# Kernel optimization log

Measured on AMD Instinct MI355X. Metric: run time of the kernel, lower is better.

## Reference

```python
import jax, jax.numpy as jnp
import numpy as np


def setup_inputs() -> dict:
    key = jax.random.key(0)
    k1, k2, k3, k4 = jax.random.split(key, 4)
    T, H, I, E, K = 4096, 1024, 1024, 8, 2
    hidden_states = jax.random.normal(k1, (T, H), dtype=jnp.float32)
    router_logits = jax.random.normal(k2, (T, E), dtype=jnp.float32)
    # fused gate+up projection: [E, H, 2*I]; down projection: [E, I, H]
    up_weight = jax.random.normal(k3, (E, H, 2 * I), dtype=jnp.float32) * 0.02
    down_weight = jax.random.normal(k4, (E, I, H), dtype=jnp.float32) * 0.02
    return {"hidden_states": hidden_states, "router_logits": router_logits,
            "up_weight": up_weight, "down_weight": down_weight, "topk": K}


def reference(hidden_states, router_logits, up_weight, down_weight, topk):
    T, H = hidden_states.shape
    E = up_weight.shape[0]
    I = down_weight.shape[1]
    K = topk
    # select_experts: softmax over all experts, top-k, renormalize weights
    probs = jax.nn.softmax(router_logits, axis=-1)
    topk_w, topk_ids = jax.lax.top_k(probs, K)               # [T, K]
    topk_w = topk_w / jnp.sum(topk_w, axis=-1, keepdims=True)
    # expand tokens: each token is dispatched K times (grouped-GEMM operand)
    xk = jnp.repeat(hidden_states, K, axis=0)                # [T*K, H]
    flat_ids = topk_ids.reshape(-1)                          # [T*K]
    acc = jnp.zeros((T * K, H), dtype=hidden_states.dtype)
    for e in range(E):  # fixed small expert loop (grouped GEMM semantics)
        mask = (flat_ids == e).astype(hidden_states.dtype)[:, None]
        xe = xk * mask                                       # zero out non-e tokens
        gu = xe @ up_weight[e]                               # [T*K, 2I]
        h = jax.nn.silu(gu[:, :I]) * gu[:, I:]               # gated SiLU
        acc = acc + h @ down_weight[e]                       # [T*K, H]
    # combine: weighted sum over the K expert slots (reduce step)
    out = jnp.einsum('tk,tkh->th', topk_w, acc.reshape(T, K, H))
    return out
```

## Files before the change

### kernel.cpp

```cpp
#include <hip/hip_runtime.h>
#include <hip/hip_bf16.h>


#define T_TOK 4096
#define HDIM  1024
#define NEXP  8
#define RROWS (T_TOK * 2)
#define MAXPE T_TOK

typedef unsigned short u16;
typedef short v8s __attribute__((ext_vector_type(8)));
typedef float v4f __attribute__((ext_vector_type(4)));
typedef __attribute__((address_space(3))) unsigned int as3_u32;
typedef const __attribute__((address_space(1))) unsigned int as1_u32c;

__device__ __forceinline__ float b2f(u16 u) {
    union { unsigned int i; float f; } v; v.i = ((unsigned int)u) << 16; return v.f;
}
__device__ __forceinline__ u16 f2b(float f) {
    union { float f; unsigned int i; } v; v.f = f;
    unsigned int x = v.i;
    return (u16)((x + 0x7FFFu + ((x >> 16) & 1u)) >> 16);
}
__device__ __forceinline__ unsigned int pack2(float a, float b) {
    return (unsigned int)f2b(a) | ((unsigned int)f2b(b) << 16);
}
__device__ __forceinline__ void stage16(const u16* g, u16* l) {
    __builtin_amdgcn_global_load_lds((as1_u32c*)g, (as3_u32*)l, 16, 0, 0);
}

__device__ __forceinline__ void cvt_tile(const float* __restrict__ Wb,
                                         u16* __restrict__ Wtb,
                                         int N, int n0b, int k0b, u16* sm) {
    const int tid = threadIdx.x;
    const int m = tid & 15, rr = tid >> 4;
    float4 f[16];
#pragma unroll
    for (int s = 0; s < 4; s++)
#pragma unroll
        for (int j = 0; j < 4; j++)
            f[s * 4 + j] = *(const float4*)(Wb + (size_t)(k0b + s * 64 + rr * 4 + j) * N
                                               + n0b + m * 4);
#pragma unroll
    for (int s = 0; s < 4; s++) {
        const int kc = s * 16 + rr;
        const float* fp = (const float*)&f[s * 4];
#pragma unroll
        for (int nl = 0; nl < 4; nl++) {
            int n_l = m * 4 + nl;
            uint2 v;
            v.x = pack2(fp[nl], fp[4 + nl]);
            v.y = pack2(fp[8 + nl], fp[12 + nl]);
            *(uint2*)&sm[n_l * 256 + ((kc ^ (n_l & 15)) << 2)] = v;
        }
    }
    __syncthreads();
    const int n_l = tid >> 2, q = tid & 3, sw = n_l & 15;
    u16* dst = Wtb + (size_t)(n0b + n_l) * 1024 + k0b + q * 64;
#pragma unroll
    for (int c2 = 0; c2 < 8; c2++) {
        uint2 a = *(const uint2*)&sm[n_l * 256 + (((q * 16 + 2 * c2) ^ sw) << 2)];
        uint2 b = *(const uint2*)&sm[n_l * 256 + (((q * 16 + 2 * c2 + 1) ^ sw) << 2)];
        uint4 o; o.x = a.x; o.y = a.y; o.z = b.x; o.w = b.y;
        *(uint4*)(dst + c2 * 8) = o;
    }
}

__global__ __launch_bounds__(256)
void prep_all(const float* __restrict__ X, const float* __restrict__ RL,
              const float* __restrict__ WU,
              u16* __restrict__ Xb, u16* __restrict__ WtU,
              int* __restrict__ ids, float* __restrict__ wts,
              int* __restrict__ counts, int* __restrict__ rowbuf) {
    __shared__ __align__(16) u16 sm[64 * 256];
    const int bx = blockIdx.x;
    const int tid = threadIdx.x;

    if (bx < 1024) {
        int e = bx >> 7, r = bx & 127;
        int nt = r >> 2, kt = r & 3;
        cvt_tile(WU + (size_t)e * 1024 * 2048, WtU + (size_t)e * 2048 * 1024,
                 2048, nt * 64, kt * 256, sm);
    } else if (bx < 1536) {
        int base = (bx - 1024) * 8192 + tid * 4;
#pragma unroll
        for (int j = 0; j < 8; j++) {
            float4 fx = *(const float4*)(X + base + j * 1024);
            uint2 o; o.x = pack2(fx.x, fx.y); o.y = pack2(fx.z, fx.w);
            *(uint2*)(Xb + base + j * 1024) = o;
        }
    } else {
        int t = (bx - 1536) * 256 + tid;
        float4 a = *(const float4*)(RL + t * NEXP);
        float4 b = *(const float4*)(RL + t * NEXP + 4);
        float l[NEXP] = {a.x, a.y, a.z, a.w, b.x, b.y, b.z, b.w};
        int i0 = 0;
#pragma unroll
        for (int q = 1; q < NEXP; q++) if (l[q] > l[i0]) i0 = q;
        int i1 = (i0 == 0) ? 1 : 0;
#pragma unroll
        for (int q = 0; q < NEXP; q++) if (q != i0 && l[q] > l[i1]) i1 = q;
        float w0 = 1.0f / (1.0f + expf(l[i1] - l[i0]));
        ids[2 * t] = i0;     ids[2 * t + 1] = i1;
        wts[2 * t] = w0;     wts[2 * t + 1] = 1.0f - w0;
        int p0 = atomicAdd(&counts[i0], 1);
        rowbuf[i0 * MAXPE + p0] = 2 * t;
        int p1 = atomicAdd(&counts[i1], 1);
        rowbuf[i1 * MAXPE + p1] = 2 * t + 1;
    }
}

template<int PHASE>
__global__ __launch_bounds__(256)
void mfma_gemm(const u16* __restrict__ A, const u16* __restrict__ Bt,
               u16* __restrict__ H,
               const int* __restrict__ counts, const int* __restrict__ rowbuf,
               const float* __restrict__ WD, u16* __restrict__ WtD) {
    __shared__ __align__(16) u16 smem[128 * 64 * 2];
    __shared__ int srid[128];
    const int bi0 = blockIdx.x;

    if (PHASE == 1 && bi0 < 512) {
        int e = bi0 >> 6, r = bi0 & 63;
        int nt = r >> 2, kt = r & 3;
        cvt_tile(WD + (size_t)e * 1024 * 1024, WtD + (size_t)e * 1024 * 1024,
                 1024, nt * 64, kt * 256, smem);
        return;
    }

    const int bi = (PHASE == 1) ? bi0 - 512 : bi0;
    const int xcd = bi & 7, kb = bi >> 3;
    int e, ct, rt;
    if (PHASE == 1) { int p = (kb & 15) * 8 + xcd; e = p >> 4; ct = p & 15; rt = kb >> 4; }
    else            { int p = (kb & 7) * 8 + xcd;  e = p >> 3; ct = p & 7;  rt = kb >> 3; }
    const int cnt = counts[e];
    if (rt * 128 >= cnt) return;
    const int tid = threadIdx.x;
    const int lane = tid & 63, wave = tid >> 6;

    u16* sA = smem;
    u16* sB = smem + 128 * 64;

    if (tid < 128) {
        int idx = rt * 128 + tid;
        srid[tid] = (idx < cnt) ? rowbuf[e * MAXPE + idx] : -1;
    }
    __syncthreads();

    const int lrow = lane >> 3;
    const int lchunk = (lane & 7) ^ lrow;
    const u16* aPtr[4]; const u16* bPtr[4];
    u16 *aDst[4], *bDst[4];
#pragma unroll
    for (int p = 0; p < 4; p++) {
        int region = p * 4 + wave;
        int r = region * 8 + lrow;
        int rid = srid[r];
        int arow = (rid < 0) ? 0 : (PHASE == 1 ? (rid >> 1) : rid);
        aPtr[p] = A + (size_t)arow * 1024 + lchunk * 8;
        aDst[p] = sA + region * 512 + lane * 8;
        int n;
        if (PHASE == 1) n = (r < 64) ? (ct * 64 + r) : (1024 + ct * 64 + (r - 64));
        else            n = ct * 128 + r;
        bPtr[p] = Bt + (size_t)e * (PHASE == 1 ? 2048 : 1024) * 1024
                     + (size_t)n * 1024 + lchunk * 8;
        bDst[p] = sB + region * 512 + lane * 8;
    }

    const int quad = lane >> 4, mr = lane & 15;
    const int swA = mr & 7;
    const v4f zf = {0.f, 0.f, 0.f, 0.f};
    v4f acc[2][8];
#pragma unroll
    for (int i = 0; i < 2; i++)
#pragma unroll
        for (int j = 0; j < 8; j++) acc[i][j] = zf;

    for (int kk = 0; kk < 16; kk++) {
        __syncthreads();
#pragma unroll
        for (int p = 0; p < 4; p++) {
            stage16(aPtr[p] + kk * 64, aDst[p]);
            stage16(bPtr[p] + kk * 64, bDst[p]);
        }
        __syncthreads();
#pragma unroll
        for (int kh = 0; kh < 2; kh++) {
            const int c = kh * 4 + quad;
            v8s a0 = *(const v8s*)(sA + (wave * 32 + mr) * 64 + ((c ^ swA) * 8));
            v8s a1 = *(const v8s*)(sA + (wave * 32 + 16 + mr) * 64 + ((c ^ swA) * 8));
#pragma unroll
            for (int nf = 0; nf < 8; nf++) {
                v8s b = *(const v8s*)(sB + (nf * 16 + mr) * 64 + ((c ^ swA) * 8));
                acc[0][nf] = __builtin_amdgcn_mfma_f32_16x16x32_bf16(a0, b, acc[0][nf], 0, 0, 0);
                acc[1][nf] = __builtin_amdgcn_mfma_f32_16x16x32_bf16(a1, b, acc[1][nf], 0, 0, 0);
            }
        }
    }

#pragma unroll
    for (int mf = 0; mf < 2; mf++) {
#pragma unroll
        for (int reg = 0; reg < 4; reg++) {
            int rl = wave * 32 + mf * 16 + quad * 4 + reg;
            int grow = srid[rl];
            if (grow < 0) continue;
            if (PHASE == 1) {
                size_t base = (size_t)grow * 1024 + ct * 64 + mr;
#pragma unroll
                for (int nf = 0; nf < 4; nf++) {
                    float g = acc[mf][nf][reg], u = acc[mf][nf + 4][reg];
                    H[base + nf * 16] = f2b((g / (1.0f + expf(-g))) * u);
                }
            } else {
                size_t base = (size_t)grow * 1024 + ct * 128 + mr;
#pragma unroll
                for (int nf = 0; nf < 8; nf++)
                    H[base + nf * 16] = f2b(acc[mf][nf][reg]);
            }
        }
    }
}

__global__ void combine_kernel(const u16* __restrict__ accb,
                               const float* __restrict__ wts,
                               float* __restrict__ out) {
    int g = blockIdx.x * blockDim.x + threadIdx.x;
    int t = g >> 8;
    int c = (g & 255) * 4;
    float w0 = wts[2 * t], w1 = wts[2 * t + 1];
    ushort4 a = *(const ushort4*)(accb + (size_t)(2 * t) * 1024 + c);
    ushort4 b = *(const ushort4*)(accb + (size_t)(2 * t + 1) * 1024 + c);
    float4 o;
    o.x = w0 * b2f(a.x) + w1 * b2f(b.x);
    o.y = w0 * b2f(a.y) + w1 * b2f(b.y);
    o.z = w0 * b2f(a.z) + w1 * b2f(b.z);
    o.w = w0 * b2f(a.w) + w1 * b2f(b.w);
    *(float4*)(out + (size_t)t * 1024 + c) = o;
}

__global__ void router_kernel(const float* __restrict__ logits,
                              int* __restrict__ ids, float* __restrict__ wts) {
    int t = blockIdx.x * blockDim.x + threadIdx.x;
    if (t >= T_TOK) return;
    float4 a = *(const float4*)(logits + t * NEXP);
    float4 b = *(const float4*)(logits + t * NEXP + 4);
    float l[NEXP] = {a.x, a.y, a.z, a.w, b.x, b.y, b.z, b.w};
    int i0 = 0;
#pragma unroll
    for (int i = 1; i < NEXP; i++) if (l[i] > l[i0]) i0 = i;
    int i1 = (i0 == 0) ? 1 : 0;
#pragma unroll
    for (int i = 0; i < NEXP; i++) if (i != i0 && l[i] > l[i1]) i1 = i;
    float w0 = 1.0f / (1.0f + expf(l[i1] - l[i0]));
    ids[2 * t] = i0;     ids[2 * t + 1] = i1;
    wts[2 * t] = w0;     wts[2 * t + 1] = 1.0f - w0;
}

__global__ void bucket_kernel(const int* __restrict__ ids,
                              int* __restrict__ counts, int* __restrict__ rowbuf) {
    int r = blockIdx.x * blockDim.x + threadIdx.x;
    if (r >= RROWS) return;
    int e = ids[r];
    int pos = atomicAdd(&counts[e], 1);
    rowbuf[e * MAXPE + pos] = r;
}

template<int GATED, int AF32>
__global__ __launch_bounds__(256)
void moe_gemm_kernel(const void* __restrict__ Av,
                     const float* __restrict__ B,
                     u16* __restrict__ C,
                     const int* __restrict__ counts,
                     const int* __restrict__ rowbuf,
                     int rowShift, int NB) {
    const int e   = blockIdx.z;
    const int cnt = counts[e];
    const int rt  = blockIdx.y;
    if (rt * 128 >= cnt) return;
    const int ct  = blockIdx.x;
    const int tid = threadIdx.x;

    __shared__ __align__(16) u16 sA[128 * 40];
    __shared__ __align__(16) u16 sB[(GATED ? 2 : 1) * 64 * 40];
    __shared__ int srid[128];

    if (tid < 128) {
        int idx = rt * 128 + tid;
        srid[tid] = (idx < cnt) ? rowbuf[e * MAXPE + idx] : -1;
    }
    __syncthreads();

    const int ar = tid >> 1, ac = (tid & 1) * 16;
    int arid = srid[ar];
    const float* aSrcF = 0; const u16* aSrcH = 0;
    if (arid >= 0) {
        if (AF32) aSrcF = (const float*)Av + (size_t)(arid >> rowShift) * HDIM + ac;
        else      aSrcH = (const u16*)Av + (size_t)(arid >> rowShift) * HDIM + ac;
    }
    u16* aDst = sA + ar * 40 + ac;

    const int kq2 = (tid >> 4) * 2, n4 = (tid & 15) * 4;
    const float* bSrcG = B + (size_t)e * 1024 * NB + (size_t)kq2 * NB + ct * 64 + n4;
    const float* bSrcU = bSrcG + 1024;

    const int lane = tid & 63, wave = tid >> 6;
    const int quad = lane >> 4, mr = lane & 15;

    const v4f zf = {0.f, 0.f, 0.f, 0.f};
    v4f accG[2][4], accU[2][4];
#pragma unroll
    for (int i = 0; i < 2; i++)
#pragma unroll
        for (int j = 0; j < 4; j++) { accG[i][j] = zf; accU[i][j] = zf; }

    for (int kk = 0; kk < HDIM / 32; kk++) {
        uint4 aw0 = make_uint4(0, 0, 0, 0), aw1 = make_uint4(0, 0, 0, 0);
        if (AF32) {
            if (aSrcF) {
                float4 f0 = *(const float4*)(aSrcF + kk * 32);
                float4 f1 = *(const float4*)(aSrcF + kk * 32 + 4);
                float4 f2 = *(const float4*)(aSrcF + kk * 32 + 8);
                float4 f3 = *(const float4*)(aSrcF + kk * 32 + 12);
                aw0 = make_uint4(pack2(f0.x, f0.y), pack2(f0.z, f0.w),
                                 pack2(f1.x, f1.y), pack2(f1.z, f1.w));
                aw1 = make_uint4(pack2(f2.x, f2.y), pack2(f2.z, f2.w),
                                 pack2(f3.x, f3.y), pack2(f3.z, f3.w));
            }
        } else {
            if (aSrcH) {
                aw0 = *(const uint4*)(aSrcH + kk * 32);
                aw1 = *(const uint4*)(aSrcH + kk * 32 + 8);
            }
        }
        const size_t bOff = (size_t)kk * 32 * NB;
        float4 g0 = *(const float4*)(bSrcG + bOff);
        float4 g1 = *(const float4*)(bSrcG + bOff + NB);
        float4 u0 = make_float4(0, 0, 0, 0), u1 = make_float4(0, 0, 0, 0);
        if (GATED) {
            u0 = *(const float4*)(bSrcU + bOff);
            u1 = *(const float4*)(bSrcU + bOff + NB);
        }

        __syncthreads();
        *(uint4*)aDst = aw0;
        *(uint4*)(aDst + 8) = aw1;
        {
            const float gx[4] = {g0.x, g0.y, g0.z, g0.w};
            const float gy[4] = {g1.x, g1.y, g1.z, g1.w};
#pragma unroll
            for (int j = 0; j < 4; j++)
                *(unsigned int*)&sB[(n4 + j) * 40 + kq2] = pack2(gx[j], gy[j]);
            if (GATED) {
                const float ux[4] = {u0.x, u0.y, u0.z, u0.w};
                const float uy[4] = {u1.x, u1.y, u1.z, u1.w};
#pragma unroll
                for (int j = 0; j < 4; j++)
                    *(unsigned int*)&sB[64 * 40 + (n4 + j) * 40 + kq2] = pack2(ux[j], uy[j]);
            }
        }
        __syncthreads();

        v8s af0 = *(const v8s*)(sA + (wave * 32 + mr) * 40 + quad * 8);
        v8s af1 = *(const v8s*)(sA + (wave * 32 + 16 + mr) * 40 + quad * 8);
#pragma unroll
        for (int nf = 0; nf < 4; nf++) {
            v8s bg = *(const v8s*)(sB + (nf * 16 + mr) * 40 + quad * 8);
            accG[0][nf] = __builtin_amdgcn_mfma_f32_16x16x32_bf16(af0, bg, accG[0][nf], 0, 0, 0);
            accG[1][nf] = __builtin_amdgcn_mfma_f32_16x16x32_bf16(af1, bg, accG[1][nf], 0, 0, 0);
            if (GATED) {
                v8s bu = *(const v8s*)(sB + 64 * 40 + (nf * 16 + mr) * 40 + quad * 8);
                accU[0][nf] = __builtin_amdgcn_mfma_f32_16x16x32_bf16(af0, bu, accU[0][nf], 0, 0, 0);
                accU[1][nf] = __builtin_amdgcn_mfma_f32_16x16x32_bf16(af1, bu, accU[1][nf], 0, 0, 0);
            }
        }
    }

#pragma unroll
    for (int mf = 0; mf < 2; mf++) {
#pragma unroll
        for (int reg = 0; reg < 4; reg++) {
            int rl = wave * 32 + mf * 16 + quad * 4 + reg;
            int grow = srid[rl];
            if (grow < 0) continue;
            size_t base = (size_t)grow * 1024 + ct * 64 + mr;
#pragma unroll
            for (int nf = 0; nf < 4; nf++) {
                float g = accG[mf][nf][reg];
                float val;
                if (GATED) {
                    float u = accU[mf][nf][reg];
                    val = (g / (1.0f + expf(-g))) * u;
                } else {
                    val = g;
                }
                C[base + nf * 16] = f2b(val);
            }
        }
    }
}

extern "C" void kernel_launch(void* const* d_in, const int* in_sizes, int n_in,
                              void* d_out, int out_size, void* d_ws, size_t ws_size,
                              hipStream_t stream) {
    const float *X = 0, *RL = 0, *WU = 0, *WD = 0;
    for (int i = 0; i < n_in; i++) {
        switch (in_sizes[i]) {
            case T_TOK * HDIM:        X  = (const float*)d_in[i]; break;
            case T_TOK * NEXP:        RL = (const float*)d_in[i]; break;
            case NEXP * HDIM * 2048:  WU = (const float*)d_in[i]; break;
            case NEXP * HDIM * 1024:  WD = (const float*)d_in[i]; break;
            default: break;
        }
    }
    if (!X)  X  = (const float*)d_in[0];
    if (!RL) RL = (const float*)d_in[1];
    if (!WU) WU = (const float*)d_in[2];
    if (!WD) WD = (const float*)d_in[3];
    float* OUT = (float*)d_out;

    char* ws = (char*)d_ws;
    int*   ids    = (int*)(ws + 0);
    float* wts    = (float*)(ws + 32768);
    int*   counts = (int*)(ws + 65536);
    int*   rowbuf = (int*)(ws + 65792);
    u16* Xb   = (u16*)(ws + 196864);
    u16* WtU  = (u16*)(ws + 8585472);
    u16* WtD  = (u16*)(ws + 42139904);
    u16* HbufF= (u16*)(ws + 58917120);
    u16* AccF = WtU;
    const size_t needFast = 75694336ull;
    u16* Hbuf = (u16*)(ws + 196864);
    u16* Acc  = (u16*)(ws + 196864 + 16777216);

    hipMemsetAsync(counts, 0, NEXP * sizeof(int), stream);

    if (ws_size >= needFast) {
        prep_all<<<1552, 256, 0, stream>>>(
            X, RL, WU, Xb, WtU, ids, wts, counts, rowbuf);
        mfma_gemm<1><<<4608, 256, 0, stream>>>(Xb, WtU, HbufF, counts, rowbuf, WD, WtD);
        mfma_gemm<2><<<2048, 256, 0, stream>>>(HbufF, WtD, AccF, counts, rowbuf,
                                               (const float*)0, (u16*)0);
        combine_kernel<<<T_TOK, 256, 0, stream>>>(AccF, wts, OUT);
    } else {
        router_kernel<<<T_TOK / 256, 256, 0, stream>>>(RL, ids, wts);
        bucket_kernel<<<RROWS / 256, 256, 0, stream>>>(ids, counts, rowbuf);
        moe_gemm_kernel<1, 1><<<dim3(16, 32, NEXP), 256, 0, stream>>>(
            (const void*)X, WU, Hbuf, counts, rowbuf, 1, 2048);
        moe_gemm_kernel<0, 0><<<dim3(16, 32, NEXP), 256, 0, stream>>>(
            (const void*)Hbuf, WD, Acc, counts, rowbuf, 0, 1024);
        combine_kernel<<<T_TOK, 256, 0, stream>>>(Acc, wts, OUT);
    }
}
```

Before: 268.9 us.

## Double-buffer GEMM LDS staging, fuse combine via atomics, interleave weight conversion

The MFMA GEMM main loop now uses two LDS buffers, so the next K-slice is staged while the current one is computed, and each K step needs one barrier instead of two. The down-projection phase scales its result by the routing weight and atomically adds it into the fp32 output, which removes the bf16 accumulator buffer and the separate combine kernel. The output is zeroed with a memset first. In phase 1, the down-weight conversion blocks are interleaved with the GEMM blocks (every ninth block) instead of all being launched up front. The cost is fp32 atomic traffic on the output and doubled LDS per block, which may lower occupancy.

Result: slower. 300.1 us (+11.6%).

```diff
diff --git a/kernel.cpp b/kernel.cpp
--- a/kernel.cpp
+++ b/kernel.cpp
@@ -115,20 +115,27 @@
 void mfma_gemm(const u16* __restrict__ A, const u16* __restrict__ Bt,
                u16* __restrict__ H,
                const int* __restrict__ counts, const int* __restrict__ rowbuf,
-               const float* __restrict__ WD, u16* __restrict__ WtD) {
-    __shared__ __align__(16) u16 smem[128 * 64 * 2];
+               const float* __restrict__ WD, u16* __restrict__ WtD,
+               const float* __restrict__ wts, float* __restrict__ out) {
+    __shared__ __align__(16) u16 smem[4 * 128 * 64];
     __shared__ int srid[128];
     const int bi0 = blockIdx.x;
 
-    if (PHASE == 1 && bi0 < 512) {
-        int e = bi0 >> 6, r = bi0 & 63;
-        int nt = r >> 2, kt = r & 3;
-        cvt_tile(WD + (size_t)e * 1024 * 1024, WtD + (size_t)e * 1024 * 1024,
-                 1024, nt * 64, kt * 256, smem);
-        return;
-    }
-
-    const int bi = (PHASE == 1) ? bi0 - 512 : bi0;
+    int bi;
+    if (PHASE == 1) {
+        if ((bi0 % 9) == 8) {
+            int ci = bi0 / 9;
+            int e = ci >> 6, r = ci & 63;
+            int nt = r >> 2, kt = r & 3;
+            cvt_tile(WD + (size_t)e * 1024 * 1024, WtD + (size_t)e * 1024 * 1024,
+                     1024, nt * 64, kt * 256, smem);
+            return;
+        }
+        bi = (bi0 / 9) * 8 + (bi0 % 9);
+    } else {
+        bi = bi0;
+    }
+
     const int xcd = bi & 7, kb = bi >> 3;
     int e, ct, rt;
     if (PHASE == 1) { int p = (kb & 15) * 8 + xcd; e = p >> 4; ct = p & 15; rt = kb >> 4; }
@@ -138,8 +145,10 @@
     const int tid = threadIdx.x;
     const int lane = tid & 63, wave = tid >> 6;
 
-    u16* sA = smem;
-    u16* sB = smem + 128 * 64;
+    u16* sA0 = smem;
+    u16* sB0 = smem + 8192;
+    u16* sA1 = smem + 16384;
+    u16* sB1 = smem + 24576;
 
     if (tid < 128) {
         int idx = rt * 128 + tid;
@@ -150,7 +159,7 @@
     const int lrow = lane >> 3;
     const int lchunk = (lane & 7) ^ lrow;
     const u16* aPtr[4]; const u16* bPtr[4];
-    u16 *aDst[4], *bDst[4];
+    int offs[4];
 #pragma unroll
     for (int p = 0; p < 4; p++) {
         int region = p * 4 + wave;
@@ -158,13 +167,12 @@
         int rid = srid[r];
         int arow = (rid < 0) ? 0 : (PHASE == 1 ? (rid >> 1) : rid);
         aPtr[p] = A + (size_t)arow * 1024 + lchunk * 8;
-        aDst[p] = sA + region * 512 + lane * 8;
         int n;
         if (PHASE == 1) n = (r < 64) ? (ct * 64 + r) : (1024 + ct * 64 + (r - 64));
         else            n = ct * 128 + r;
         bPtr[p] = Bt + (size_t)e * (PHASE == 1 ? 2048 : 1024) * 1024
                      + (size_t)n * 1024 + lchunk * 8;
-        bDst[p] = sB + region * 512 + lane * 8;
+        offs[p] = region * 512 + lane * 8;
     }
 
     const int quad = lane >> 4, mr = lane & 15;
@@ -176,26 +184,38 @@
 #pragma unroll
         for (int j = 0; j < 8; j++) acc[i][j] = zf;
 
-    for (int kk = 0; kk < 16; kk++) {
-        __syncthreads();
+    auto stageAll = [&](u16* sAx, u16* sBx, int kk) {
 #pragma unroll
         for (int p = 0; p < 4; p++) {
-            stage16(aPtr[p] + kk * 64, aDst[p]);
-            stage16(bPtr[p] + kk * 64, bDst[p]);
-        }
-        __syncthreads();
+            stage16(aPtr[p] + kk * 64, sAx + offs[p]);
+            stage16(bPtr[p] + kk * 64, sBx + offs[p]);
+        }
+    };
+    auto computeTile = [&](const u16* sAx, const u16* sBx) {
 #pragma unroll
         for (int kh = 0; kh < 2; kh++) {
             const int c = kh * 4 + quad;
-            v8s a0 = *(const v8s*)(sA + (wave * 32 + mr) * 64 + ((c ^ swA) * 8));
-            v8s a1 = *(const v8s*)(sA + (wave * 32 + 16 + mr) * 64 + ((c ^ swA) * 8));
+            v8s a0 = *(const v8s*)(sAx + (wave * 32 + mr) * 64 + ((c ^ swA) * 8));
+            v8s a1 = *(const v8s*)(sAx + (wave * 32 + 16 + mr) * 64 + ((c ^ swA) * 8));
 #pragma unroll
             for (int nf = 0; nf < 8; nf++) {
-                v8s b = *(const v8s*)(sB + (nf * 16 + mr) * 64 + ((c ^ swA) * 8));
+                v8s b = *(const v8s*)(sBx + (nf * 16 + mr) * 64 + ((c ^ swA) * 8));
                 acc[0][nf] = __builtin_amdgcn_mfma_f32_16x16x32_bf16(a0, b, acc[0][nf], 0, 0, 0);
                 acc[1][nf] = __builtin_amdgcn_mfma_f32_16x16x32_bf16(a1, b, acc[1][nf], 0, 0, 0);
             }
         }
+    };
+
+    stageAll(sA0, sB0, 0);
+    __syncthreads();
+#pragma unroll 1
+    for (int kt = 0; kt < 8; kt++) {
+        stageAll(sA1, sB1, 2 * kt + 1);
+        computeTile(sA0, sB0);
+        __syncthreads();
+        if (kt < 7) stageAll(sA0, sB0, 2 * kt + 2);
+        computeTile(sA1, sB1);
+        __syncthreads();
     }
 
 #pragma unroll
@@ -213,10 +233,11 @@
                     H[base + nf * 16] = f2b((g / (1.0f + expf(-g))) * u);
                 }
             } else {
-                size_t base = (size_t)grow * 1024 + ct * 128 + mr;
+                float w = wts[grow];
+                float* ob = out + (size_t)(grow >> 1) * 1024 + ct * 128 + mr;
 #pragma unroll
                 for (int nf = 0; nf < 8; nf++)
-                    H[base + nf * 16] = f2b(acc[mf][nf][reg]);
+                    atomicAdd(ob + nf * 16, w * acc[mf][nf][reg]);
             }
         }
     }
@@ -428,7 +449,6 @@
     u16* WtU  = (u16*)(ws + 8585472);
     u16* WtD  = (u16*)(ws + 42139904);
     u16* HbufF= (u16*)(ws + 58917120);
-    u16* AccF = WtU;
     const size_t needFast = 75694336ull;
     u16* Hbuf = (u16*)(ws + 196864);
     u16* Acc  = (u16*)(ws + 196864 + 16777216);
@@ -436,12 +456,13 @@
     hipMemsetAsync(counts, 0, NEXP * sizeof(int), stream);
 
     if (ws_size >= needFast) {
+        hipMemsetAsync(OUT, 0, (size_t)T_TOK * HDIM * sizeof(float), stream);
         prep_all<<<1552, 256, 0, stream>>>(
             X, RL, WU, Xb, WtU, ids, wts, counts, rowbuf);
-        mfma_gemm<1><<<4608, 256, 0, stream>>>(Xb, WtU, HbufF, counts, rowbuf, WD, WtD);
-        mfma_gemm<2><<<2048, 256, 0, stream>>>(HbufF, WtD, AccF, counts, rowbuf,
-                                               (const float*)0, (u16*)0);
-        combine_kernel<<<T_TOK, 256, 0, stream>>>(AccF, wts, OUT);
+        mfma_gemm<1><<<4608, 256, 0, stream>>>(Xb, WtU, HbufF, counts, rowbuf,
+                                               WD, WtD, (const float*)0, (float*)0);
+        mfma_gemm<2><<<2048, 256, 0, stream>>>(HbufF, WtD, (u16*)0, counts, rowbuf,
+                                               (const float*)0, (u16*)0, wts, OUT);
     } else {
         router_kernel<<<T_TOK / 256, 256, 0, stream>>>(RL, ids, wts);
         bucket_kernel<<<RROWS / 256, 256, 0, stream>>>(ids, counts, rowbuf);
```
